# Kernel optimization log

Hardware: AMD Instinct MI355X
Metric: run time of the kernel (lower is better)

The kernel has to match this reference:

```python
import jax, jax.numpy as jnp
import numpy as np

BATCH = 8
IN_FEATURES = 4096
OUT_FEATURES = 16384


def setup_inputs() -> dict:
    key = jax.random.key(0)
    k1, k2, k3 = jax.random.split(key, 3)
    # activations, fp16 (w4a16 path)
    x = jax.random.normal(k1, (BATCH, IN_FEATURES), dtype=jnp.float16)
    # packed int4 weights: each element holds two signed 4-bit values
    # (low nibble = even column 2k, high nibble = odd column 2k+1)
    weight = jax.random.randint(k2, (OUT_FEATURES, IN_FEATURES // 2), 0, 256, dtype=jnp.int32)
    # per-output-channel symmetric scales (small positive values)
    weight_scales = (jax.random.uniform(k3, (OUT_FEATURES,), dtype=jnp.float16) * jnp.float16(0.01)
                     + jnp.float16(0.001))
    return {"x": x, "weight": weight, "weight_scales": weight_scales}


def _dequant_i4(weight, scales):
    """Unpack two signed int4 per byte and apply per-row scales.
    weight: [out, in//2] int32 (byte values 0..255); scales: [out] fp16.
    Returns [out, in] in scales.dtype.
    """
    low = weight & 0xF
    high = (weight >> 4) & 0xF
    # sign-extend 4-bit two's complement (the torch module stores signed int4;
    # mask 0x88 XOR in the kernel is the equivalent sign-bit flip)
    low = jnp.where(low >= 8, low - 16, low)
    high = jnp.where(high >= 8, high - 16, high)
    w = jnp.stack([low, high], axis=-1).reshape(weight.shape[0], -1)  # [out, in]
    return w.astype(scales.dtype) * scales[:, None]


def reference(x, weight, weight_scales):
    W = _dequant_i4(weight, weight_scales)           # [out, in] fp16
    return jnp.matmul(x, W.T)                         # [batch, out] fp16
```

## Files before the change

### kernel.cpp

```cpp
#include <hip/hip_runtime.h>
#include <hip/hip_bf16.h>
#include <stdint.h>

#define BATCH 8
#define K_DIM 4096
#define N_DIM 16384
#define KH (K_DIM / 2)
#define BLOCK 512
#define ROWS_PER_WAVE 4
#define ROWS_PER_BLOCK 32
#define ITERS (KH / 4 / 64)

__device__ __forceinline__ float bf16lo(uint32_t u) { return __uint_as_float(u << 16); }
__device__ __forceinline__ float bf16hi(uint32_t u) { return __uint_as_float(u & 0xFFFF0000u); }

__device__ __forceinline__ uint32_t f32_to_bf16_bits(float f) {
    uint32_t u = __float_as_uint(f);
    return (u + 0x7FFFu + ((u >> 16) & 1u)) >> 16;
}

__global__ __launch_bounds__(BLOCK, 2)
void w4a16_gemv(const float* __restrict__ x,
                const int*   __restrict__ w,
                const float* __restrict__ scales,
                float*       __restrict__ out)
{
    __shared__ uint4 xchunks[K_DIM];
    const int tid = threadIdx.x;

    #pragma unroll
    for (int t = 0; t < K_DIM / BLOCK; ++t) {
        const int c = t * BLOCK + tid;
        float v[BATCH];
        #pragma unroll
        for (int b = 0; b < BATCH; ++b) v[b] = x[b * K_DIM + c];
        uint4 pk;
        pk.x = f32_to_bf16_bits(v[0]) | (f32_to_bf16_bits(v[1]) << 16);
        pk.y = f32_to_bf16_bits(v[2]) | (f32_to_bf16_bits(v[3]) << 16);
        pk.z = f32_to_bf16_bits(v[4]) | (f32_to_bf16_bits(v[5]) << 16);
        pk.w = f32_to_bf16_bits(v[6]) | (f32_to_bf16_bits(v[7]) << 16);
        xchunks[c ^ ((c >> 3) & 7)] = pk;
    }
    __syncthreads();

    const int wave = tid >> 6;
    const int lane = tid & 63;
    const int row0 = blockIdx.x * ROWS_PER_BLOCK + wave * ROWS_PER_WAVE;

    const int4* __restrict__ wv0 = (const int4*)(w + (size_t)(row0 + 0) * KH);
    const int4* __restrict__ wv1 = (const int4*)(w + (size_t)(row0 + 1) * KH);
    const int4* __restrict__ wv2 = (const int4*)(w + (size_t)(row0 + 2) * KH);
    const int4* __restrict__ wv3 = (const int4*)(w + (size_t)(row0 + 3) * KH);

    float acc[ROWS_PER_WAVE][BATCH];
    #pragma unroll
    for (int j = 0; j < ROWS_PER_WAVE; ++j)
        #pragma unroll
        for (int b = 0; b < BATCH; ++b) acc[j][b] = 0.0f;

    #pragma unroll 1
    for (int t = 0; t < ITERS; ++t) {
        const int u = (t << 6) + lane;
        int4 q0 = wv0[u];
        int4 q1 = wv1[u];
        int4 q2 = wv2[u];
        int4 q3 = wv3[u];
        const int xork  = u & 7;
        const int cbase = u << 3;

        int qw[ROWS_PER_WAVE][4];
        qw[0][0] = q0.x; qw[0][1] = q0.y; qw[0][2] = q0.z; qw[0][3] = q0.w;
        qw[1][0] = q1.x; qw[1][1] = q1.y; qw[1][2] = q1.z; qw[1][3] = q1.w;
        qw[2][0] = q2.x; qw[2][1] = q2.y; qw[2][2] = q2.z; qw[2][3] = q2.w;
        qw[3][0] = q3.x; qw[3][1] = q3.y; qw[3][2] = q3.z; qw[3][3] = q3.w;

        #pragma unroll
        for (int m = 0; m < 4; ++m) {
            const uint4 xa = xchunks[cbase + ((2 * m)     ^ xork)];
            const uint4 xb = xchunks[cbase + ((2 * m + 1) ^ xork)];

            float xlo[BATCH], xhi[BATCH];
            xlo[0] = bf16lo(xa.x); xlo[1] = bf16hi(xa.x);
            xlo[2] = bf16lo(xa.y); xlo[3] = bf16hi(xa.y);
            xlo[4] = bf16lo(xa.z); xlo[5] = bf16hi(xa.z);
            xlo[6] = bf16lo(xa.w); xlo[7] = bf16hi(xa.w);
            xhi[0] = bf16lo(xb.x); xhi[1] = bf16hi(xb.x);
            xhi[2] = bf16lo(xb.y); xhi[3] = bf16hi(xb.y);
            xhi[4] = bf16lo(xb.z); xhi[5] = bf16hi(xb.z);
            xhi[6] = bf16lo(xb.w); xhi[7] = bf16hi(xb.w);

            #pragma unroll
            for (int j = 0; j < ROWS_PER_WAVE; ++j) {
                const unsigned bv = ((unsigned)qw[j][m]) & 0xFFu;
                const float flo = (float)((int)((bv & 0xFu) ^ 8u) - 8);
                const float fhi = (float)((int)(((bv >> 4) & 0xFu) ^ 8u) - 8);
                #pragma unroll
                for (int b = 0; b < BATCH; ++b) {
                    acc[j][b] = fmaf(flo, xlo[b], acc[j][b]);
                    acc[j][b] = fmaf(fhi, xhi[b], acc[j][b]);
                }
            }
        }
    }

    float vals[32];
    #pragma unroll
    for (int j = 0; j < ROWS_PER_WAVE; ++j)
        #pragma unroll
        for (int b = 0; b < BATCH; ++b) vals[j * 8 + b] = acc[j][b];

    #pragma unroll
    for (int k = 0; k < 5; ++k) {
        const int sel = (lane >> k) & 1;
        const int n = 32 >> k;
        #pragma unroll
        for (int i = 0; i < n / 2; ++i) {
            const float a = vals[2 * i];
            const float c = vals[2 * i + 1];
            const float mine  = sel ? c : a;
            const float other = sel ? a : c;
            vals[i] = mine + __shfl_xor(other, 1 << k, 64);
        }
    }
    const float total = vals[0] + __shfl_xor(vals[0], 32, 64);

    if (lane < 32) {
        const int r = row0 + (lane >> 3);
        out[(size_t)(lane & 7) * N_DIM + r] = total * scales[r];
    }
}

extern "C" void kernel_launch(void* const* d_in, const int* in_sizes, int n_in,
                              void* d_out, int out_size, void* d_ws, size_t ws_size,
                              hipStream_t stream) {
    const float* x      = (const float*)d_in[0];
    const int*   w      = (const int*)d_in[1];
    const float* scales = (const float*)d_in[2];
    float*       out    = (float*)d_out;

    dim3 grid(N_DIM / ROWS_PER_BLOCK);
    dim3 block(BLOCK);
    hipLaunchKernelGGL(w4a16_gemv, grid, block, 0, stream, x, w, scales, out);
}
```

Before: 198.4 us.

## Use fp16 packed dot2 with magic-number int4 dequant and register prefetch

```diff
diff --git a/kernel.cpp b/kernel.cpp
--- a/kernel.cpp
+++ b/kernel.cpp
@@ -1,45 +1,50 @@
 #include <hip/hip_runtime.h>
-#include <hip/hip_bf16.h>
 #include <stdint.h>
 
 #define BATCH 8
 #define K_DIM 4096
 #define N_DIM 16384
 #define KH (K_DIM / 2)
+#define NPAIR (K_DIM / 2)
 #define BLOCK 512
 #define ROWS_PER_WAVE 4
 #define ROWS_PER_BLOCK 32
 #define ITERS (KH / 4 / 64)
 
-__device__ __forceinline__ float bf16lo(uint32_t u) { return __uint_as_float(u << 16); }
-__device__ __forceinline__ float bf16hi(uint32_t u) { return __uint_as_float(u & 0xFFFF0000u); }
+typedef _Float16 h2 __attribute__((ext_vector_type(2)));
+typedef int i4 __attribute__((ext_vector_type(4)));
 
-__device__ __forceinline__ uint32_t f32_to_bf16_bits(float f) {
-    uint32_t u = __float_as_uint(f);
-    return (u + 0x7FFFu + ((u >> 16) & 1u)) >> 16;
+__device__ __forceinline__ h2 as_h2(uint32_t u) { return __builtin_bit_cast(h2, u); }
+
+__device__ __forceinline__ float fdot2f(h2 a, h2 b, float c) {
+#if __has_builtin(__builtin_amdgcn_fdot2)
+    return __builtin_amdgcn_fdot2(a, b, c, false);
+#else
+    return fmaf((float)a[1], (float)b[1], fmaf((float)a[0], (float)b[0], c));
+#endif
 }
 
-__global__ __launch_bounds__(BLOCK, 2)
+__global__ __launch_bounds__(BLOCK, 4)
 void w4a16_gemv(const float* __restrict__ x,
                 const int*   __restrict__ w,
                 const float* __restrict__ scales,
                 float*       __restrict__ out)
 {
-    __shared__ uint4 xchunks[K_DIM];
+    __shared__ uint4 xchunks[2 * NPAIR];
     const int tid = threadIdx.x;
 
     #pragma unroll
-    for (int t = 0; t < K_DIM / BLOCK; ++t) {
-        const int c = t * BLOCK + tid;
-        float v[BATCH];
+    for (int it = 0; it < NPAIR / BLOCK; ++it) {
+        const int p = it * BLOCK + tid;
+        uint32_t pk[BATCH];
         #pragma unroll
-        for (int b = 0; b < BATCH; ++b) v[b] = x[b * K_DIM + c];
-        uint4 pk;
-        pk.x = f32_to_bf16_bits(v[0]) | (f32_to_bf16_bits(v[1]) << 16);
-        pk.y = f32_to_bf16_bits(v[2]) | (f32_to_bf16_bits(v[3]) << 16);
-        pk.z = f32_to_bf16_bits(v[4]) | (f32_to_bf16_bits(v[5]) << 16);
-        pk.w = f32_to_bf16_bits(v[6]) | (f32_to_bf16_bits(v[7]) << 16);
-        xchunks[c ^ ((c >> 3) & 7)] = pk;
+        for (int b = 0; b < BATCH; ++b) {
+            const float2 v = *reinterpret_cast<const float2*>(x + (size_t)b * K_DIM + 2 * p);
+            pk[b] = __builtin_bit_cast(uint32_t, __builtin_amdgcn_cvt_pkrtz(v.x, v.y));
+        }
+        const int c0 = 2 * p, c1 = 2 * p + 1;
+        xchunks[c0 ^ ((c0 >> 3) & 7)] = make_uint4(pk[0], pk[1], pk[2], pk[3]);
+        xchunks[c1 ^ ((c1 >> 3) & 7)] = make_uint4(pk[4], pk[5], pk[6], pk[7]);
     }
     __syncthreads();
 
@@ -47,10 +52,10 @@
     const int lane = tid & 63;
     const int row0 = blockIdx.x * ROWS_PER_BLOCK + wave * ROWS_PER_WAVE;
 
-    const int4* __restrict__ wv0 = (const int4*)(w + (size_t)(row0 + 0) * KH);
-    const int4* __restrict__ wv1 = (const int4*)(w + (size_t)(row0 + 1) * KH);
-    const int4* __restrict__ wv2 = (const int4*)(w + (size_t)(row0 + 2) * KH);
-    const int4* __restrict__ wv3 = (const int4*)(w + (size_t)(row0 + 3) * KH);
+    const i4* __restrict__ wv0 = (const i4*)(w + (size_t)(row0 + 0) * KH);
+    const i4* __restrict__ wv1 = (const i4*)(w + (size_t)(row0 + 1) * KH);
+    const i4* __restrict__ wv2 = (const i4*)(w + (size_t)(row0 + 2) * KH);
+    const i4* __restrict__ wv3 = (const i4*)(w + (size_t)(row0 + 3) * KH);
 
     float acc[ROWS_PER_WAVE][BATCH];
     #pragma unroll
@@ -58,50 +63,59 @@
         #pragma unroll
         for (int b = 0; b < BATCH; ++b) acc[j][b] = 0.0f;
 
-    #pragma unroll 1
-    for (int t = 0; t < ITERS; ++t) {
+    const h2 neg1032 = as_h2(0xE408E408u);
+
+    int qw[4][4];
+    {
+        const i4 a = __builtin_nontemporal_load(wv0 + lane);
+        const i4 b = __builtin_nontemporal_load(wv1 + lane);
+        const i4 c = __builtin_nontemporal_load(wv2 + lane);
+        const i4 d = __builtin_nontemporal_load(wv3 + lane);
+        qw[0][0] = a[0]; qw[0][1] = a[1]; qw[0][2] = a[2]; qw[0][3] = a[3];
+        qw[1][0] = b[0]; qw[1][1] = b[1]; qw[1][2] = b[2]; qw[1][3] = b[3];
+        qw[2][0] = c[0]; qw[2][1] = c[1]; qw[2][2] = c[2]; qw[2][3] = c[3];
+        qw[3][0] = d[0]; qw[3][1] = d[1]; qw[3][2] = d[2]; qw[3][3] = d[3];
+    }
+
+    auto compute = [&](int t) {
         const int u = (t << 6) + lane;
-        int4 q0 = wv0[u];
-        int4 q1 = wv1[u];
-        int4 q2 = wv2[u];
-        int4 q3 = wv3[u];
-        const int xork  = u & 7;
         const int cbase = u << 3;
-
-        int qw[ROWS_PER_WAVE][4];
-        qw[0][0] = q0.x; qw[0][1] = q0.y; qw[0][2] = q0.z; qw[0][3] = q0.w;
-        qw[1][0] = q1.x; qw[1][1] = q1.y; qw[1][2] = q1.z; qw[1][3] = q1.w;
-        qw[2][0] = q2.x; qw[2][1] = q2.y; qw[2][2] = q2.z; qw[2][3] = q2.w;
-        qw[3][0] = q3.x; qw[3][1] = q3.y; qw[3][2] = q3.z; qw[3][3] = q3.w;
-
+        const int xork = u & 7;
         #pragma unroll
         for (int m = 0; m < 4; ++m) {
             const uint4 xa = xchunks[cbase + ((2 * m)     ^ xork)];
             const uint4 xb = xchunks[cbase + ((2 * m + 1) ^ xork)];
-
-            float xlo[BATCH], xhi[BATCH];
-            xlo[0] = bf16lo(xa.x); xlo[1] = bf16hi(xa.x);
-            xlo[2] = bf16lo(xa.y); xlo[3] = bf16hi(xa.y);
-            xlo[4] = bf16lo(xa.z); xlo[5] = bf16hi(xa.z);
-            xlo[6] = bf16lo(xa.w); xlo[7] = bf16hi(xa.w);
-            xhi[0] = bf16lo(xb.x); xhi[1] = bf16hi(xb.x);
-            xhi[2] = bf16lo(xb.y); xhi[3] = bf16hi(xb.y);
-            xhi[4] = bf16lo(xb.z); xhi[5] = bf16hi(xb.z);
-            xhi[6] = bf16lo(xb.w); xhi[7] = bf16hi(xb.w);
-
             #pragma unroll
             for (int j = 0; j < ROWS_PER_WAVE; ++j) {
-                const unsigned bv = ((unsigned)qw[j][m]) & 0xFFu;
-                const float flo = (float)((int)((bv & 0xFu) ^ 8u) - 8);
-                const float fhi = (float)((int)(((bv >> 4) & 0xFu) ^ 8u) - 8);
-                #pragma unroll
-                for (int b = 0; b < BATCH; ++b) {
-                    acc[j][b] = fmaf(flo, xlo[b], acc[j][b]);
-                    acc[j][b] = fmaf(fhi, xhi[b], acc[j][b]);
-                }
+                const uint32_t bv = (uint32_t)qw[j][m];
+                const uint32_t tt = (bv & 0xFu) | ((bv << 12) & 0x000F0000u);
+                const h2 w2 = as_h2(tt ^ 0x64086408u) + neg1032;
+                acc[j][0] = fdot2f(w2, as_h2(xa.x), acc[j][0]);
+                acc[j][1] = fdot2f(w2, as_h2(xa.y), acc[j][1]);
+                acc[j][2] = fdot2f(w2, as_h2(xa.z), acc[j][2]);
+                acc[j][3] = fdot2f(w2, as_h2(xa.w), acc[j][3]);
+                acc[j][4] = fdot2f(w2, as_h2(xb.x), acc[j][4]);
+                acc[j][5] = fdot2f(w2, as_h2(xb.y), acc[j][5]);
+                acc[j][6] = fdot2f(w2, as_h2(xb.z), acc[j][6]);
+                acc[j][7] = fdot2f(w2, as_h2(xb.w), acc[j][7]);
             }
         }
+    };
+
+    #pragma unroll 1
+    for (int t = 0; t < ITERS - 1; ++t) {
+        const int un = ((t + 1) << 6) + lane;
+        const i4 a = __builtin_nontemporal_load(wv0 + un);
+        const i4 b = __builtin_nontemporal_load(wv1 + un);
+        const i4 c = __builtin_nontemporal_load(wv2 + un);
+        const i4 d = __builtin_nontemporal_load(wv3 + un);
+        compute(t);
+        qw[0][0] = a[0]; qw[0][1] = a[1]; qw[0][2] = a[2]; qw[0][3] = a[3];
+        qw[1][0] = b[0]; qw[1][1] = b[1]; qw[1][2] = b[2]; qw[1][3] = b[3];
+        qw[2][0] = c[0]; qw[2][1] = c[1]; qw[2][2] = c[2]; qw[2][3] = c[3];
+        qw[3][0] = d[0]; qw[3][1] = d[1]; qw[3][2] = d[2]; qw[3][3] = d[3];
     }
+    compute(ITERS - 1);
 
     float vals[32];
     #pragma unroll
```

Measured after the change: 194.2 us. 2.1% less time.
